# Kernel tuning notes

Hardware: AMD Instinct MI355X
Metric: run time of the kernel (lower is better)

Reference implementation:

```python
import jax, jax.numpy as jnp
import numpy as np

HIDDEN = 768
N_HEADS = 12
HEAD_DIM = HIDDEN // N_HEADS  # 64 (multihead=True)
NEG_BIG = -1e31


def setup_inputs() -> dict:
    key = jax.random.key(0)
    ks = jax.random.split(key, 8)
    B, S = 4, 2048
    toks = jax.random.normal(ks[0], (B, S, HIDDEN), dtype=jnp.float32)
    masks = jax.random.randint(ks[1], (B, S), 0, 2, dtype=jnp.int32)
    s = 0.02
    Wq = jax.random.normal(ks[2], (HIDDEN, HIDDEN), dtype=jnp.float32) * s
    Wk = jax.random.normal(ks[3], (HIDDEN, HIDDEN), dtype=jnp.float32) * s
    Wv = jax.random.normal(ks[4], (HIDDEN, HIDDEN), dtype=jnp.float32) * s
    bq = jax.random.normal(ks[5], (HIDDEN,), dtype=jnp.float32) * s
    bk = jax.random.normal(ks[6], (HIDDEN,), dtype=jnp.float32) * s
    bv = jax.random.normal(ks[7], (HIDDEN,), dtype=jnp.float32) * s
    return {"toks": toks, "masks": masks, "Wq": Wq, "bq": bq,
            "Wk": Wk, "bk": bk, "Wv": Wv, "bv": bv}


def reference(toks, masks, Wq, bq, Wk, bk, Wv, bv):
    B, S, D = toks.shape
    m = masks.astype(jnp.float32)  # [B,S]
    # additive outer-product padding mask: (1 - m_i*m_j) * -1e31, shape [B,S,S]
    add_mask = (1.0 - m[:, :, None] * m[:, None, :]) * NEG_BIG

    def split_heads(x):  # [B,S,D] -> [B,H,S,hd]
        return x.reshape(B, S, N_HEADS, HEAD_DIM).transpose(0, 2, 1, 3)

    q = split_heads(toks @ Wq + bq)
    k = split_heads(toks @ Wk + bk)
    v = split_heads(toks @ Wv + bv)

    scores = jnp.einsum("bhqd,bhkd->bhqk", q, k) / jnp.sqrt(
        jnp.asarray(HEAD_DIM, dtype=toks.dtype))
    scores = scores + add_mask[:, None, :, :]
    probs = jax.nn.softmax(scores, axis=-1)  # dropout is identity at eval
    ctx = jnp.einsum("bhqk,bhkd->bhqd", probs, v)
    return ctx.transpose(0, 2, 1, 3).reshape(B, S, D)
```

## Files before the change

kernel.cpp:

```cpp
#include <hip/hip_runtime.h>
#include <hip/hip_bf16.h>
#include <cstddef>


typedef __bf16 bf16_8 __attribute__((ext_vector_type(8)));
typedef float f32x4 __attribute__((ext_vector_type(4)));
typedef short s16x4 __attribute__((ext_vector_type(4)));
typedef short s16x8 __attribute__((ext_vector_type(8)));

#define HID 768
#define NHEADS 12
#define HD 64
#define BATCH 4
#define SEQ 2048
#define NEGBIG2 (-1.44269504e31f)
#define SCALE2 0.18033688f

#define KT 64
#define NKT (SEQ / KT)
#define STR 68
#define ASTR 40

static __device__ __forceinline__ f32x4 mfma16x16x32(bf16_8 a, bf16_8 b, f32x4 c) {
  return __builtin_amdgcn_mfma_f32_16x16x32_bf16(a, b, c, 0, 0, 0);
}

static __device__ __forceinline__ void lds_barrier() {
  __asm__ volatile("s_waitcnt lgkmcnt(0)\n\ts_barrier" ::: "memory");
}

static __device__ __forceinline__ void lds_flush() {
  __asm__ volatile("s_waitcnt lgkmcnt(0)" ::: "memory");
}

static __device__ __forceinline__ float fast_exp2(float x) {
#if __has_builtin(__builtin_amdgcn_exp2f)
  return __builtin_amdgcn_exp2f(x);
#else
  return __expf(x * 0.69314718f);
#endif
}

static __device__ __forceinline__ s16x4 pack_bf16x4(f32x4 p) {
  s16x4 o;
#pragma unroll
  for (int i = 0; i < 4; ++i) {
    __bf16 b = (__bf16)p[i];
    o[i] = __builtin_bit_cast(short, b);
  }
  return o;
}

static __device__ __forceinline__ bf16_8 cat2(const __bf16* p) {
  s16x4 lo = *(const s16x4*)p;
  s16x4 hi = *(const s16x4*)(p + 4);
  s16x8 v = __builtin_shufflevector(lo, hi, 0, 1, 2, 3, 4, 5, 6, 7);
  return __builtin_bit_cast(bf16_8, v);
}

static __device__ __forceinline__ void write2(__bf16* p, s16x8 v) {
  *(s16x4*)p = __builtin_shufflevector(v, v, 0, 1, 2, 3);
  *(s16x4*)(p + 4) = __builtin_shufflevector(v, v, 4, 5, 6, 7);
}

static __device__ __forceinline__ bf16_8 cvt_a_frag(const float* p) {
  f32x4 af0 = *(const f32x4*)p;
  f32x4 af1 = *(const f32x4*)(p + 4);
  bf16_8 a;
  a[0] = (__bf16)af0[0]; a[1] = (__bf16)af0[1];
  a[2] = (__bf16)af0[2]; a[3] = (__bf16)af0[3];
  a[4] = (__bf16)af1[0]; a[5] = (__bf16)af1[1];
  a[6] = (__bf16)af1[2]; a[7] = (__bf16)af1[3];
  return a;
}

__global__ __launch_bounds__(256) void mask_kadd(const int* __restrict__ masks,
                                                 float* __restrict__ kaddG) {
  int i = blockIdx.x * 256 + threadIdx.x;
  kaddG[i] = masks[i] ? 0.0f : NEGBIG2;
}

__global__ __launch_bounds__(256) void transpose768x3(const float* __restrict__ Wq,
                                                      const float* __restrict__ Wk,
                                                      const float* __restrict__ Wv,
                                                      __bf16* __restrict__ WtBase) {
  const float* in = blockIdx.z == 0 ? Wq : (blockIdx.z == 1 ? Wk : Wv);
  __bf16* out = WtBase + (size_t)blockIdx.z * HID * HID;
  __shared__ __bf16 tile[32][33];
  int bx = blockIdx.x * 32, by = blockIdx.y * 32;
  int tx = threadIdx.x, ty = threadIdx.y;
#pragma unroll
  for (int r = 0; r < 32; r += 8)
    tile[ty + r][tx] = (__bf16)in[(size_t)(by + ty + r) * HID + bx + tx];
  __syncthreads();
#pragma unroll
  for (int r = 0; r < 32; r += 8)
    out[(size_t)(bx + ty + r) * HID + by + tx] = tile[tx][ty + r];
}

__global__ __launch_bounds__(256, 4) void proj_kv(const float* __restrict__ toks,
                                                  const __bf16* __restrict__ WtK,
                                                  const float* __restrict__ bk,
                                                  const __bf16* __restrict__ WtV,
                                                  const float* __restrict__ bv,
                                                  __bf16* __restrict__ Kout,
                                                  __bf16* __restrict__ Vtout,
                                                  int head0, int hm) {
  __shared__ __align__(16) __bf16 ldsA[2][64 * ASTR];
  int tid = threadIdx.x;
  int w = tid >> 6, lane = tid & 63, l16 = lane & 15, quad = lane >> 4;
  int m0 = blockIdx.x * 64;
  int hl = blockIdx.y, h = head0 + hl;
  int srow = tid >> 2, scg = tid & 3;
  const float* asrc = toks + (size_t)(m0 + srow) * HID + scg * 8;
  const __bf16* bKrow = WtK + (size_t)(h * 64 + w * 16 + l16) * HID + quad * 8;
  const __bf16* bVrow = WtV + (size_t)(h * 64 + w * 16 + l16) * HID + quad * 8;
  f32x4 zero = {0.f, 0.f, 0.f, 0.f};
  f32x4 aK[4], aV[4];
#pragma unroll
  for (int mt = 0; mt < 4; ++mt) { aK[mt] = zero; aV[mt] = zero; }

  *(bf16_8*)(&ldsA[0][srow * ASTR + scg * 8]) = cvt_a_frag(asrc);
  __syncthreads();

  const int NCH = HID / 32;
  for (int t = 0; t < NCH; ++t) {
    int b = t & 1;
    int kk = t * 32;
    bf16_8 areg;
    if (t + 1 < NCH) areg = cvt_a_frag(asrc + kk + 32);
    bf16_8 bkf = *(const bf16_8*)(bKrow + kk);
    bf16_8 bvf = *(const bf16_8*)(bVrow + kk);
#pragma unroll
    for (int mt = 0; mt < 4; ++mt) {
      bf16_8 af = *(const bf16_8*)(&ldsA[b][(mt * 16 + l16) * ASTR + quad * 8]);
      aK[mt] = mfma16x16x32(af, bkf, aK[mt]);
      aV[mt] = mfma16x16x32(af, bvf, aV[mt]);
    }
    if (t + 1 < NCH) {
      *(bf16_8*)(&ldsA[b ^ 1][srow * ASTR + scg * 8]) = areg;
      lds_barrier();
    }
  }

  int d = w * 16 + l16;
  float bnK = bk[h * 64 + d];
  float bnV = bv[h * 64 + d];
#pragma unroll
  for (int mt = 0; mt < 4; ++mt) {
#pragma unroll
    for (int r = 0; r < 4; ++r) {
      int m = m0 + mt * 16 + quad * 4 + r;
      int b = m >> 11;
      int s = m & (SEQ - 1);
      Kout[(((size_t)b * hm + hl) * SEQ + s) * HD + d] = (__bf16)(aK[mt][r] + bnK);
      Vtout[(((size_t)b * hm + hl) * HD + d) * SEQ + s] = (__bf16)(aV[mt][r] + bnV);
    }
  }
}

__global__ __launch_bounds__(256, 3) void attn_fused(const float* __restrict__ toks,
                                                     const __bf16* __restrict__ WtQ,
                                                     const float* __restrict__ bq,
                                                     const __bf16* __restrict__ Kbuf,
                                                     const __bf16* __restrict__ Vtbuf,
                                                     const float* __restrict__ kaddG,
                                                     float* __restrict__ out,
                                                     int head0, int hm) {
  __shared__ __align__(16) __bf16 ldsK[2][64 * STR];
  __shared__ __align__(16) __bf16 ldsV[2][64 * STR];
  __shared__ __align__(16) __bf16 ldsQP[64 * STR];
  int tid = threadIdx.x;
  int w = tid >> 6, lane = tid & 63, l16 = lane & 15, quad = lane >> 4;

  int nwg = gridDim.x * gridDim.y * gridDim.z;
  int hwf = blockIdx.x + gridDim.x * (blockIdx.y + gridDim.y * blockIdx.z);
  int lg = (hwf & 7) * (nwg >> 3) + (hwf >> 3);
  int q0 = (lg & (gridDim.x - 1)) * 64;
  int grp = lg / gridDim.x;
  int hl = grp % hm, bz = grp / hm;
  int h = head0 + hl;

  const float* kb = kaddG + (size_t)bz * SEQ;
  f32x4 zero = {0.f, 0.f, 0.f, 0.f};

  const __bf16* Kb = Kbuf + ((size_t)bz * hm + hl) * SEQ * HD;
  const __bf16* Vb = Vtbuf + ((size_t)bz * hm + hl) * HD * SEQ;
  __bf16* Pw = &ldsQP[(w * 16) * STR];

  {
    const float* arow = toks + ((size_t)bz * SEQ + q0 + w * 16 + l16) * HID + quad * 8;
    const __bf16* brow = WtQ + (size_t)(h * 64 + l16) * HID + quad * 8;
    f32x4 qa[4] = {zero, zero, zero, zero};
    for (int kk = 0; kk < HID; kk += 32) {
      bf16_8 a = cvt_a_frag(arow + kk);
#pragma unroll
      for (int t = 0; t < 4; ++t)
        qa[t] = mfma16x16x32(a, *(const bf16_8*)(brow + (size_t)t * 16 * HID + kk), qa[t]);
    }
#pragma unroll
    for (int t = 0; t < 4; ++t) {
      float bn = bq[h * 64 + t * 16 + l16];
#pragma unroll
      for (int r = 0; r < 4; ++r)
        Pw[(quad * 4 + r) * STR + t * 16 + l16] = (__bf16)(qa[t][r] + bn);
    }
  }
  lds_flush();

  bf16_8 qf[2];
#pragma unroll
  for (int half = 0; half < 2; ++half)
    qf[half] = cat2(&Pw[l16 * STR + half * 32 + quad * 8]);
  float actq = (kb[q0 + w * 16 + l16] == 0.0f) ? 1.0f : 0.0f;

  int srow = tid >> 3, sc = tid & 7;
  {
    s16x8 k0 = *(const s16x8*)(Kb + (size_t)srow * HD + sc * 8);
    s16x8 k1 = *(const s16x8*)(Kb + (size_t)(srow + 32) * HD + sc * 8);
    s16x8 v0 = *(const s16x8*)(Vb + (size_t)srow * SEQ + sc * 8);
    s16x8 v1 = *(const s16x8*)(Vb + (size_t)(srow + 32) * SEQ + sc * 8);
    write2(&ldsK[0][srow * STR + sc * 8], k0);
    write2(&ldsK[0][(srow + 32) * STR + sc * 8], k1);
    write2(&ldsV[0][srow * STR + sc * 8], v0);
    write2(&ldsV[0][(srow + 32) * STR + sc * 8], v1);
  }
  s16x8 kA0 = *(const s16x8*)(Kb + (size_t)(KT + srow) * HD + sc * 8);
  s16x8 kA1 = *(const s16x8*)(Kb + (size_t)(KT + srow + 32) * HD + sc * 8);
  s16x8 vA0 = *(const s16x8*)(Vb + (size_t)srow * SEQ + KT + sc * 8);
  s16x8 vA1 = *(const s16x8*)(Vb + (size_t)(srow + 32) * SEQ + KT + sc * 8);
  s16x8 kB0, kB1, vB0, vB1;
  lds_barrier();

  float lsum = 0.f;
  f32x4 acc[4];
#pragma unroll
  for (int dt = 0; dt < 4; ++dt) acc[dt] = zero;

  auto body = [&](int buf, int t) __attribute__((always_inline)) {
    int j0 = t * KT;
#pragma unroll
    for (int kbk = 0; kbk < 4; ++kbk) {
      bf16_8 kf0 = cat2(&ldsK[buf][(kbk * 16 + l16) * STR + quad * 8]);
      bf16_8 kf1 = cat2(&ldsK[buf][(kbk * 16 + l16) * STR + 32 + quad * 8]);
      f32x4 st = mfma16x16x32(kf1, qf[1], mfma16x16x32(kf0, qf[0], zero));
      f32x4 ck = *(const f32x4*)(kb + j0 + kbk * 16 + quad * 4);
      f32x4 p;
#pragma unroll
      for (int r = 0; r < 4; ++r) {
        float v = actq * fmaf(st[r], SCALE2, ck[r]);
        p[r] = fast_exp2(v);
      }
      lsum += p[0] + p[1] + p[2] + p[3];
      *(s16x4*)(&Pw[l16 * STR + kbk * 16 + quad * 4]) = pack_bf16x4(p);
    }
    lds_flush();
#pragma unroll
    for (int kc = 0; kc < 2; ++kc) {
      bf16_8 pf = cat2(&Pw[l16 * STR + kc * 32 + quad * 8]);
#pragma unroll
      for (int dt = 0; dt < 4; ++dt) {
        bf16_8 vf = cat2(&ldsV[buf][(dt * 16 + l16) * STR + kc * 32 + quad * 8]);
        acc[dt] = mfma16x16x32(pf, vf, acc[dt]);
      }
    }
  };

  for (int t = 0; t < NKT; t += 2) {
    {
      int j2 = (t + 2 < NKT) ? (t + 2) * KT : 0;
      kB0 = *(const s16x8*)(Kb + (size_t)(j2 + srow) * HD + sc * 8);
      kB1 = *(const s16x8*)(Kb + (size_t)(j2 + srow + 32) * HD + sc * 8);
      vB0 = *(const s16x8*)(Vb + (size_t)srow * SEQ + j2 + sc * 8);
      vB1 = *(const s16x8*)(Vb + (size_t)(srow + 32) * SEQ + j2 + sc * 8);
    }
    body(0, t);
    write2(&ldsK[1][srow * STR + sc * 8], kA0);
    write2(&ldsK[1][(srow + 32) * STR + sc * 8], kA1);
    write2(&ldsV[1][srow * STR + sc * 8], vA0);
    write2(&ldsV[1][(srow + 32) * STR + sc * 8], vA1);
    lds_barrier();
    {
      int j3 = (t + 3 < NKT) ? (t + 3) * KT : 0;
      kA0 = *(const s16x8*)(Kb + (size_t)(j3 + srow) * HD + sc * 8);
      kA1 = *(const s16x8*)(Kb + (size_t)(j3 + srow + 32) * HD + sc * 8);
      vA0 = *(const s16x8*)(Vb + (size_t)srow * SEQ + j3 + sc * 8);
      vA1 = *(const s16x8*)(Vb + (size_t)(srow + 32) * SEQ + j3 + sc * 8);
    }
    body(1, t + 1);
    write2(&ldsK[0][srow * STR + sc * 8], kB0);
    write2(&ldsK[0][(srow + 32) * STR + sc * 8], kB1);
    write2(&ldsV[0][srow * STR + sc * 8], vB0);
    write2(&ldsV[0][(srow + 32) * STR + sc * 8], vB1);
    lds_barrier();
  }

  float v = lsum;
  v += __shfl_xor(v, 16);
  v += __shfl_xor(v, 32);
  float linv = 1.0f / v;
  float lr[4];
#pragma unroll
  for (int r = 0; r < 4; ++r) lr[r] = __shfl(linv, quad * 4 + r);
#pragma unroll
  for (int dt = 0; dt < 4; ++dt)
#pragma unroll
    for (int r = 0; r < 4; ++r)
      out[((size_t)bz * SEQ + q0 + w * 16 + quad * 4 + r) * HID + h * HD + dt * 16 + l16] =
          acc[dt][r] * lr[r];
}

extern "C" void kernel_launch(void* const* d_in, const int* in_sizes, int n_in,
                              void* d_out, int out_size, void* d_ws, size_t ws_size,
                              hipStream_t stream) {
  (void)in_sizes; (void)n_in; (void)out_size;
  const float* toks = (const float*)d_in[0];
  const int* masks = (const int*)d_in[1];
  const float* Wq = (const float*)d_in[2];
  const float* bq = (const float*)d_in[3];
  const float* Wk = (const float*)d_in[4];
  const float* bk = (const float*)d_in[5];
  const float* Wv = (const float*)d_in[6];
  const float* bv = (const float*)d_in[7];
  char* ws = (char*)d_ws;
  const size_t KADD_B = (size_t)BATCH * SEQ * 4;
  const size_t WT_B = (size_t)HID * HID * 2;
  const size_t KV_FULL_B = (size_t)BATCH * NHEADS * SEQ * HD * 2;
  const size_t KV_HEAD_B = (size_t)BATCH * SEQ * HD * 2;
  const size_t TIER_A_NEED = KADD_B + 3 * WT_B + 2 * KV_FULL_B;
  float* kaddG = (float*)(ws);
  __bf16* WtQ = (__bf16*)(ws + KADD_B + 0 * WT_B);
  __bf16* WtK = (__bf16*)(ws + KADD_B + 1 * WT_B);
  __bf16* WtV = (__bf16*)(ws + KADD_B + 2 * WT_B);
  float* outp = (float*)d_out;

  mask_kadd<<<BATCH * SEQ / 256, 256, 0, stream>>>(masks, kaddG);
  dim3 tgrid(HID / 32, HID / 32, 3), tblk(32, 8);
  transpose768x3<<<tgrid, tblk, 0, stream>>>(Wq, Wk, Wv, WtQ);

  if (ws_size >= TIER_A_NEED) {
    __bf16* Kf = (__bf16*)(ws + KADD_B + 3 * WT_B);
    __bf16* Vtf = (__bf16*)(ws + KADD_B + 3 * WT_B + KV_FULL_B);
    dim3 pgrid(BATCH * SEQ / 64, NHEADS);
    proj_kv<<<pgrid, 256, 0, stream>>>(toks, WtK, bk, WtV, bv, Kf, Vtf, 0, NHEADS);
    dim3 agrid(SEQ / 64, NHEADS, BATCH);
    attn_fused<<<agrid, 256, 0, stream>>>(toks, WtQ, bq, Kf, Vtf, kaddG, outp, 0, NHEADS);
  } else {
    __bf16* Kh = (__bf16*)(ws + KADD_B + 3 * WT_B);
    __bf16* Vth = (__bf16*)(ws + KADD_B + 3 * WT_B + KV_HEAD_B);
    dim3 pgrid(BATCH * SEQ / 64, 1);
    dim3 agrid(SEQ / 64, 1, BATCH);
    for (int h = 0; h < NHEADS; ++h) {
      proj_kv<<<pgrid, 256, 0, stream>>>(toks, WtK, bk, WtV, bv, Kh, Vth, h, 1);
      attn_fused<<<agrid, 256, 0, stream>>>(toks, WtQ, bq, Kh, Vth, kaddG, outp, h, 1);
    }
  }
}
```

Measured before the change: 308.9 us.

## Switch attention to 32x32x16 MFMA with 128-query tiles and register-resident P

The attention kernel now gives each wave 32 query rows (128 per workgroup) and computes scores and P·V with 32x32x16 bf16 MFMA instead of 16x16x32. The probabilities are packed to bf16 and rearranged across lane halves with v_permlane32_swap, so they feed the PV MFMA directly from registers and no longer round-trip through LDS. Each K/V tile load is reused by twice as many queries. The trade-offs are half as many workgroups in the grid, larger accumulator register pressure, and a more complex lane mapping for the output writes.

```diff
diff --git a/kernel.cpp b/kernel.cpp
--- a/kernel.cpp
+++ b/kernel.cpp
@@ -5,8 +5,10 @@
 
 typedef __bf16 bf16_8 __attribute__((ext_vector_type(8)));
 typedef float f32x4 __attribute__((ext_vector_type(4)));
+typedef float f32x16 __attribute__((ext_vector_type(16)));
 typedef short s16x4 __attribute__((ext_vector_type(4)));
 typedef short s16x8 __attribute__((ext_vector_type(8)));
+typedef unsigned int u32x4 __attribute__((ext_vector_type(4)));
 
 #define HID 768
 #define NHEADS 12
@@ -16,21 +18,24 @@
 #define NEGBIG2 (-1.44269504e31f)
 #define SCALE2 0.18033688f
 
-#define KT 64
-#define NKT (SEQ / KT)
+#define KVB 64
+#define NKT (SEQ / KVB)
 #define STR 68
 #define ASTR 40
 
 static __device__ __forceinline__ f32x4 mfma16x16x32(bf16_8 a, bf16_8 b, f32x4 c) {
   return __builtin_amdgcn_mfma_f32_16x16x32_bf16(a, b, c, 0, 0, 0);
 }
+static __device__ __forceinline__ f32x16 mfma32x32x16(bf16_8 a, bf16_8 b, f32x16 c) {
+  return __builtin_amdgcn_mfma_f32_32x32x16_bf16(a, b, c, 0, 0, 0);
+}
+
+static __device__ __forceinline__ void pl32swap(unsigned& a, unsigned& b) {
+  asm("v_permlane32_swap_b32 %0, %1" : "+v"(a), "+v"(b));
+}
 
 static __device__ __forceinline__ void lds_barrier() {
   __asm__ volatile("s_waitcnt lgkmcnt(0)\n\ts_barrier" ::: "memory");
-}
-
-static __device__ __forceinline__ void lds_flush() {
-  __asm__ volatile("s_waitcnt lgkmcnt(0)" ::: "memory");
 }
 
 static __device__ __forceinline__ float fast_exp2(float x) {
@@ -41,14 +46,10 @@
 #endif
 }
 
-static __device__ __forceinline__ s16x4 pack_bf16x4(f32x4 p) {
-  s16x4 o;
-#pragma unroll
-  for (int i = 0; i < 4; ++i) {
-    __bf16 b = (__bf16)p[i];
-    o[i] = __builtin_bit_cast(short, b);
-  }
-  return o;
+static __device__ __forceinline__ unsigned pkbf(float a, float b) {
+  unsigned lo = (unsigned)__builtin_bit_cast(unsigned short, (__bf16)a);
+  unsigned hi = (unsigned)__builtin_bit_cast(unsigned short, (__bf16)b);
+  return lo | (hi << 16);
 }
 
 static __device__ __forceinline__ bf16_8 cat2(const __bf16* p) {
@@ -167,16 +168,17 @@
                                                      const float* __restrict__ kaddG,
                                                      float* __restrict__ out,
                                                      int head0, int hm) {
-  __shared__ __align__(16) __bf16 ldsK[2][64 * STR];
-  __shared__ __align__(16) __bf16 ldsV[2][64 * STR];
-  __shared__ __align__(16) __bf16 ldsQP[64 * STR];
+  __shared__ __align__(16) __bf16 ldsK[2][KVB * STR];
+  __shared__ __align__(16) __bf16 ldsV[2][HD * STR];
+  __shared__ __align__(16) __bf16 ldsQ[128 * STR];
   int tid = threadIdx.x;
   int w = tid >> 6, lane = tid & 63, l16 = lane & 15, quad = lane >> 4;
+  int l32 = lane & 31, hi = lane >> 5;
 
   int nwg = gridDim.x * gridDim.y * gridDim.z;
   int hwf = blockIdx.x + gridDim.x * (blockIdx.y + gridDim.y * blockIdx.z);
   int lg = (hwf & 7) * (nwg >> 3) + (hwf >> 3);
-  int q0 = (lg & (gridDim.x - 1)) * 64;
+  int q0 = (lg & (gridDim.x - 1)) * 128;
   int grp = lg / gridDim.x;
   int hl = grp % hm, bz = grp / hm;
   int h = head0 + hl;
@@ -186,10 +188,18 @@
 
   const __bf16* Kb = Kbuf + ((size_t)bz * hm + hl) * SEQ * HD;
   const __bf16* Vb = Vtbuf + ((size_t)bz * hm + hl) * HD * SEQ;
-  __bf16* Pw = &ldsQP[(w * 16) * STR];
-
-  {
-    const float* arow = toks + ((size_t)bz * SEQ + q0 + w * 16 + l16) * HID + quad * 8;
+  __bf16* Qw = &ldsQ[(w * 32) * STR];
+
+  int srow = tid >> 3, sc = tid & 7;
+  s16x8 k00 = *(const s16x8*)(Kb + (size_t)srow * HD + sc * 8);
+  s16x8 k01 = *(const s16x8*)(Kb + (size_t)(srow + 32) * HD + sc * 8);
+  s16x8 v00 = *(const s16x8*)(Vb + (size_t)srow * SEQ + sc * 8);
+  s16x8 v01 = *(const s16x8*)(Vb + (size_t)(srow + 32) * SEQ + sc * 8);
+
+#pragma unroll
+  for (int qs = 0; qs < 2; ++qs) {
+    const float* arow =
+        toks + ((size_t)bz * SEQ + q0 + w * 32 + qs * 16 + l16) * HID + quad * 8;
     const __bf16* brow = WtQ + (size_t)(h * 64 + l16) * HID + quad * 8;
     f32x4 qa[4] = {zero, zero, zero, zero};
     for (int kk = 0; kk < HID; kk += 32) {
@@ -203,72 +213,80 @@
       float bn = bq[h * 64 + t * 16 + l16];
 #pragma unroll
       for (int r = 0; r < 4; ++r)
-        Pw[(quad * 4 + r) * STR + t * 16 + l16] = (__bf16)(qa[t][r] + bn);
-    }
-  }
-  lds_flush();
-
-  bf16_8 qf[2];
-#pragma unroll
-  for (int half = 0; half < 2; ++half)
-    qf[half] = cat2(&Pw[l16 * STR + half * 32 + quad * 8]);
-  float actq = (kb[q0 + w * 16 + l16] == 0.0f) ? 1.0f : 0.0f;
-
-  int srow = tid >> 3, sc = tid & 7;
-  {
-    s16x8 k0 = *(const s16x8*)(Kb + (size_t)srow * HD + sc * 8);
-    s16x8 k1 = *(const s16x8*)(Kb + (size_t)(srow + 32) * HD + sc * 8);
-    s16x8 v0 = *(const s16x8*)(Vb + (size_t)srow * SEQ + sc * 8);
-    s16x8 v1 = *(const s16x8*)(Vb + (size_t)(srow + 32) * SEQ + sc * 8);
-    write2(&ldsK[0][srow * STR + sc * 8], k0);
-    write2(&ldsK[0][(srow + 32) * STR + sc * 8], k1);
-    write2(&ldsV[0][srow * STR + sc * 8], v0);
-    write2(&ldsV[0][(srow + 32) * STR + sc * 8], v1);
-  }
-  s16x8 kA0 = *(const s16x8*)(Kb + (size_t)(KT + srow) * HD + sc * 8);
-  s16x8 kA1 = *(const s16x8*)(Kb + (size_t)(KT + srow + 32) * HD + sc * 8);
-  s16x8 vA0 = *(const s16x8*)(Vb + (size_t)srow * SEQ + KT + sc * 8);
-  s16x8 vA1 = *(const s16x8*)(Vb + (size_t)(srow + 32) * SEQ + KT + sc * 8);
+        Qw[(qs * 16 + quad * 4 + r) * STR + t * 16 + l16] = (__bf16)(qa[t][r] + bn);
+    }
+  }
+
+  write2(&ldsK[0][srow * STR + sc * 8], k00);
+  write2(&ldsK[0][(srow + 32) * STR + sc * 8], k01);
+  write2(&ldsV[0][srow * STR + sc * 8], v00);
+  write2(&ldsV[0][(srow + 32) * STR + sc * 8], v01);
+  s16x8 kA0 = *(const s16x8*)(Kb + (size_t)(KVB + srow) * HD + sc * 8);
+  s16x8 kA1 = *(const s16x8*)(Kb + (size_t)(KVB + srow + 32) * HD + sc * 8);
+  s16x8 vA0 = *(const s16x8*)(Vb + (size_t)srow * SEQ + KVB + sc * 8);
+  s16x8 vA1 = *(const s16x8*)(Vb + (size_t)(srow + 32) * SEQ + KVB + sc * 8);
   s16x8 kB0, kB1, vB0, vB1;
   lds_barrier();
 
+  bf16_8 qf[4];
+#pragma unroll
+  for (int c = 0; c < 4; ++c)
+    qf[c] = cat2(&Qw[l32 * STR + c * 16 + hi * 8]);
+  float actq = (kb[q0 + w * 32 + l32] == 0.0f) ? 1.0f : 0.0f;
+
   float lsum = 0.f;
-  f32x4 acc[4];
-#pragma unroll
-  for (int dt = 0; dt < 4; ++dt) acc[dt] = zero;
+  f32x16 acc0, acc1;
+#pragma unroll
+  for (int i = 0; i < 16; ++i) { acc0[i] = 0.f; acc1[i] = 0.f; }
 
   auto body = [&](int buf, int t) __attribute__((always_inline)) {
-    int j0 = t * KT;
-#pragma unroll
-    for (int kbk = 0; kbk < 4; ++kbk) {
-      bf16_8 kf0 = cat2(&ldsK[buf][(kbk * 16 + l16) * STR + quad * 8]);
-      bf16_8 kf1 = cat2(&ldsK[buf][(kbk * 16 + l16) * STR + 32 + quad * 8]);
-      f32x4 st = mfma16x16x32(kf1, qf[1], mfma16x16x32(kf0, qf[0], zero));
-      f32x4 ck = *(const f32x4*)(kb + j0 + kbk * 16 + quad * 4);
-      f32x4 p;
-#pragma unroll
-      for (int r = 0; r < 4; ++r) {
-        float v = actq * fmaf(st[r], SCALE2, ck[r]);
-        p[r] = fast_exp2(v);
+    int j0 = t * KVB;
+#pragma unroll
+    for (int s = 0; s < 2; ++s) {
+      f32x16 st;
+#pragma unroll
+      for (int i = 0; i < 16; ++i) st[i] = 0.f;
+#pragma unroll
+      for (int c = 0; c < 4; ++c) {
+        bf16_8 kf = cat2(&ldsK[buf][(s * 32 + l32) * STR + c * 16 + hi * 8]);
+        st = mfma32x32x16(kf, qf[c], st);
       }
-      lsum += p[0] + p[1] + p[2] + p[3];
-      *(s16x4*)(&Pw[l16 * STR + kbk * 16 + quad * 4]) = pack_bf16x4(p);
-    }
-    lds_flush();
-#pragma unroll
-    for (int kc = 0; kc < 2; ++kc) {
-      bf16_8 pf = cat2(&Pw[l16 * STR + kc * 32 + quad * 8]);
-#pragma unroll
-      for (int dt = 0; dt < 4; ++dt) {
-        bf16_8 vf = cat2(&ldsV[buf][(dt * 16 + l16) * STR + kc * 32 + quad * 8]);
-        acc[dt] = mfma16x16x32(pf, vf, acc[dt]);
+      unsigned wds[8];
+#pragma unroll
+      for (int g = 0; g < 4; ++g) {
+        f32x4 ck = *(const f32x4*)(kb + j0 + s * 32 + g * 8 + hi * 4);
+        float p0 = fast_exp2(actq * fmaf(st[g * 4 + 0], SCALE2, ck[0]));
+        float p1 = fast_exp2(actq * fmaf(st[g * 4 + 1], SCALE2, ck[1]));
+        float p2 = fast_exp2(actq * fmaf(st[g * 4 + 2], SCALE2, ck[2]));
+        float p3 = fast_exp2(actq * fmaf(st[g * 4 + 3], SCALE2, ck[3]));
+        lsum += p0 + p1 + p2 + p3;
+        wds[g * 2] = pkbf(p0, p1);
+        wds[g * 2 + 1] = pkbf(p2, p3);
+      }
+      pl32swap(wds[0], wds[2]);
+      pl32swap(wds[1], wds[3]);
+      pl32swap(wds[4], wds[6]);
+      pl32swap(wds[5], wds[7]);
+      u32x4 pd0 = {wds[0], wds[1], wds[2], wds[3]};
+      u32x4 pd1 = {wds[4], wds[5], wds[6], wds[7]};
+      bf16_8 pa0 = __builtin_bit_cast(bf16_8, pd0);
+      bf16_8 pa1 = __builtin_bit_cast(bf16_8, pd1);
+      {
+        bf16_8 vf00 = cat2(&ldsV[buf][(0 * 32 + l32) * STR + s * 32 + hi * 8]);
+        bf16_8 vf01 = cat2(&ldsV[buf][(0 * 32 + l32) * STR + s * 32 + 16 + hi * 8]);
+        acc0 = mfma32x32x16(pa0, vf00, acc0);
+        acc0 = mfma32x32x16(pa1, vf01, acc0);
+        bf16_8 vf10 = cat2(&ldsV[buf][(1 * 32 + l32) * STR + s * 32 + hi * 8]);
+        bf16_8 vf11 = cat2(&ldsV[buf][(1 * 32 + l32) * STR + s * 32 + 16 + hi * 8]);
+        acc1 = mfma32x32x16(pa0, vf10, acc1);
+        acc1 = mfma32x32x16(pa1, vf11, acc1);
       }
     }
   };
 
   for (int t = 0; t < NKT; t += 2) {
     {
-      int j2 = (t + 2 < NKT) ? (t + 2) * KT : 0;
+      int j2 = (t + 2 < NKT) ? (t + 2) * KVB : 0;
       kB0 = *(const s16x8*)(Kb + (size_t)(j2 + srow) * HD + sc * 8);
       kB1 = *(const s16x8*)(Kb + (size_t)(j2 + srow + 32) * HD + sc * 8);
       vB0 = *(const s16x8*)(Vb + (size_t)srow * SEQ + j2 + sc * 8);
@@ -281,7 +299,7 @@
     write2(&ldsV[1][(srow + 32) * STR + sc * 8], vA1);
     lds_barrier();
     {
-      int j3 = (t + 3 < NKT) ? (t + 3) * KT : 0;
+      int j3 = (t + 3 < NKT) ? (t + 3) * KVB : 0;
       kA0 = *(const s16x8*)(Kb + (size_t)(j3 + srow) * HD + sc * 8);
       kA1 = *(const s16x8*)(Kb + (size_t)(j3 + srow + 32) * HD + sc * 8);
       vA0 = *(const s16x8*)(Vb + (size_t)srow * SEQ + j3 + sc * 8);
@@ -296,18 +314,16 @@
   }
 
   float v = lsum;
-  v += __shfl_xor(v, 16);
   v += __shfl_xor(v, 32);
   float linv = 1.0f / v;
-  float lr[4];
-#pragma unroll
-  for (int r = 0; r < 4; ++r) lr[r] = __shfl(linv, quad * 4 + r);
-#pragma unroll
-  for (int dt = 0; dt < 4; ++dt)
-#pragma unroll
-    for (int r = 0; r < 4; ++r)
-      out[((size_t)bz * SEQ + q0 + w * 16 + quad * 4 + r) * HID + h * HD + dt * 16 + l16] =
-          acc[dt][r] * lr[r];
+#pragma unroll
+  for (int r = 0; r < 16; ++r) {
+    int row = (r & 3) + 8 * (r >> 2) + 4 * hi;
+    float sc2 = __shfl(linv, row);
+    size_t orow = (size_t)bz * SEQ + q0 + w * 32 + row;
+    out[orow * HID + h * HD + l32] = acc0[r] * sc2;
+    out[orow * HID + h * HD + 32 + l32] = acc1[r] * sc2;
+  }
 }
 
 extern "C" void kernel_launch(void* const* d_in, const int* in_sizes, int n_in,
@@ -343,13 +359,13 @@
     __bf16* Vtf = (__bf16*)(ws + KADD_B + 3 * WT_B + KV_FULL_B);
     dim3 pgrid(BATCH * SEQ / 64, NHEADS);
     proj_kv<<<pgrid, 256, 0, stream>>>(toks, WtK, bk, WtV, bv, Kf, Vtf, 0, NHEADS);
-    dim3 agrid(SEQ / 64, NHEADS, BATCH);
+    dim3 agrid(SEQ / 128, NHEADS, BATCH);
     attn_fused<<<agrid, 256, 0, stream>>>(toks, WtQ, bq, Kf, Vtf, kaddG, outp, 0, NHEADS);
   } else {
     __bf16* Kh = (__bf16*)(ws + KADD_B + 3 * WT_B);
     __bf16* Vth = (__bf16*)(ws + KADD_B + 3 * WT_B + KV_HEAD_B);
     dim3 pgrid(BATCH * SEQ / 64, 1);
-    dim3 agrid(SEQ / 64, 1, BATCH);
+    dim3 agrid(SEQ / 128, 1, BATCH);
     for (int h = 0; h < NHEADS; ++h) {
       proj_kv<<<pgrid, 256, 0, stream>>>(toks, WtK, bk, WtV, bv, Kh, Vth, h, 1);
       attn_fused<<<agrid, 256, 0, stream>>>(toks, WtQ, bq, Kh, Vth, kaddG, outp, h, 1);
```

New measurement: 317.4 us. +2.8%, slower.
